# Kernel tuning notes

Measured on AMD Instinct MI355X. Metric: run time of the kernel, lower is better.

The kernel has to match this reference:

```python
import jax, jax.numpy as jnp
import numpy as np

BETA = 0.25


def setup_inputs() -> dict:
    key = jax.random.key(0)
    k1, k2 = jax.random.split(key)
    z = jax.random.normal(k1, (16, 256, 32, 32), dtype=jnp.float32)
    # nn.Embedding init: uniform(-1/K, 1/K) with K = in_channels = 16384
    K, D = 16384, 256
    emb = jax.random.uniform(k2, (K, D), dtype=jnp.float32,
                             minval=-1.0 / K, maxval=1.0 / K)
    return {"z": z, "emb": emb}


def reference(z, emb):
    K, D = emb.shape
    # NCHW -> NHWC, flatten to tokens
    zp = jnp.transpose(z, (0, 2, 3, 1))            # [B,H,W,D]
    zf = zp.reshape(-1, D)                          # [N,D]
    # squared L2 distances: ||z||^2 + ||e||^2 - 2 z.e  -> [N,K]
    d = (jnp.sum(zf * zf, axis=1, keepdims=True)
         + jnp.sum(emb * emb, axis=1)
         - 2.0 * jnp.matmul(zf, emb.T))
    idx = jnp.argmin(d, axis=1)                     # [N] int
    # gather via direct lookup (equivalent to one-hot @ emb)
    z_q = emb[idx].reshape(zp.shape)                # [B,H,W,D]
    # commitment + codebook loss
    loss = (jnp.mean((jax.lax.stop_gradient(z_q) - zp) ** 2)
            + BETA * jnp.mean((z_q - jax.lax.stop_gradient(zp)) ** 2))
    # perplexity from code usage histogram (same as mean of one-hot rows)
    counts = jax.ops.segment_sum(jnp.ones_like(idx, dtype=jnp.float32), idx,
                                 num_segments=K)
    e_mean = counts / idx.shape[0]
    perplexity = jnp.exp(-jnp.sum(e_mean * jnp.log(e_mean + 1e-10)))
    # straight-through estimator, back to NCHW
    z_q_st = zp + jax.lax.stop_gradient(z_q - zp)
    z_q_out = jnp.transpose(z_q_st, (0, 3, 1, 2))   # [B,D,H,W]
    return z_q_out, loss, perplexity, idx
```

## Files before the change

### kernel.cpp

```cpp
#include <hip/hip_runtime.h>
#include <math.h>

#define NTOK   16384
#define DDIM   256
#define HWD    1024
#define CHW    262144
#define MARGIN 3.0e-4f
#define CLIPF  5.5f
#define QS     (127.0f/5.5f)
#define EQS    2080768.0f
#define SCALE  (5.5f/(127.0f*127.0f*16384.0f))

#define WS_TI8   0u
#define WS_CI8   4194304u
#define WS_M1    8388608u
#define WS_M2    16777216u
#define WS_ARG   25165824u
#define WS_FLG   29360128u
#define WS_EE    29376512u
#define WS_ZZ    29442048u
#define WS_IDX   29507584u
#define WS_CNT   29573120u
#define WS_SUM   29638656u

typedef __attribute__((ext_vector_type(4)))  int   i32x4;
typedef __attribute__((ext_vector_type(16))) char  c16;

__device__ __forceinline__ void top2m(int& a1, int& a2, const int b1, const int b2) {
  const int mn = min(a1, b1);
  a1 = max(a1, b1);
  a2 = max(max(a2, b2), mn);
}

__global__ __launch_bounds__(256) void k_prep(const float* __restrict__ z,
                                              const float* __restrict__ emb,
                                              char* __restrict__ Ti8,
                                              char* __restrict__ Ci8,
                                              float* __restrict__ zz,
                                              float* __restrict__ ee,
                                              float* __restrict__ zt,
                                              unsigned char* __restrict__ flags) {
  const int bid = blockIdx.x;
  const int tid = threadIdx.x;
  const int t64 = tid & 63, chunk = tid >> 6;
  if (bid < 256) {
    __shared__ double part[4][64];
    __shared__ int   fpart[4][64];
    const int n = bid * 64 + t64;
    const int b = n >> 10, hw = n & 1023;
    const float* zp = z + (size_t)b * CHW + hw;
    float tmp[64];
    double s = 0.0;
    int clip = 0;
    #pragma unroll
    for (int j = 0; j < 64; ++j) {
      const float f = zp[(size_t)(chunk * 64 + j) * HWD];
      tmp[j] = f;
      s += (double)f * (double)f;
      clip |= (fabsf(f) > CLIPF) ? 1 : 0;
    }
    c16 q[4];
    #pragma unroll
    for (int sl = 0; sl < 4; ++sl)
      #pragma unroll
      for (int j = 0; j < 16; ++j)
        q[sl][j] = (char)(int)rintf(fminf(fmaxf(tmp[sl * 16 + j], -CLIPF), CLIPF) * QS);
    const int rl = n & 127, tile = n >> 7;
    char* dst = Ti8 + (size_t)tile * 32768 + chunk * 8192 + rl * 64;
    const int sw = ((rl >> 1) & 3) << 4;
    #pragma unroll
    for (int sl = 0; sl < 4; ++sl) *(c16*)(dst + ((sl * 16) ^ sw)) = q[sl];
    float* ztp = zt + (size_t)n * 256 + chunk * 64;
    #pragma unroll
    for (int j4 = 0; j4 < 16; ++j4) *(float4*)(ztp + j4 * 4) = *(float4*)&tmp[j4 * 4];
    part[chunk][t64] = s;
    fpart[chunk][t64] = clip;
    __syncthreads();
    if (tid < 64) {
      zz[n] = (float)(part[0][t64] + part[1][t64] + part[2][t64] + part[3][t64]);
      flags[n] = (unsigned char)(fpart[0][t64] | fpart[1][t64] | fpart[2][t64] | fpart[3][t64]);
    }
  } else {
    __shared__ float rows[64][257];
    __shared__ double part2[4][64];
    const int k0 = (bid - 256) * 64;
    for (int i = tid; i < 16384; i += 256)
      rows[i >> 8][i & 255] = emb[(size_t)k0 * DDIM + i];
    __syncthreads();
    const int code = k0 + t64;
    double s = 0.0;
    c16 q[4];
    #pragma unroll
    for (int sl = 0; sl < 4; ++sl)
      #pragma unroll
      for (int j = 0; j < 16; ++j) {
        const float f = rows[t64][chunk * 64 + sl * 16 + j];
        q[sl][j] = (char)(int)rintf(f * EQS);
        s += (double)f * (double)f;
      }
    char* dst = Ci8 + (size_t)code * 256 + chunk * 64;
    #pragma unroll
    for (int sl = 0; sl < 4; ++sl) *(c16*)(dst + sl * 16) = q[sl];
    part2[chunk][t64] = s;
    __syncthreads();
    if (tid < 64)
      ee[code] = (float)(part2[0][t64] + part2[1][t64] + part2[2][t64] + part2[3][t64]);
  }
}

__global__ __launch_bounds__(256) void k_mdist(
    const char* __restrict__ tokimg, const char* __restrict__ codrows,
    _Float16* __restrict__ M1, _Float16* __restrict__ M2,
    unsigned char* __restrict__ ARG) {
  __shared__ __attribute__((aligned(16))) char ldsB[65536];
  __shared__ _Float16 m1l[256];
  __shared__ _Float16 m2l[256];
  __shared__ unsigned char agl[256];
  const int raw = blockIdx.x;
  const int p = raw & 7;
  const int ctile = p * 16 + ((raw >> 3) & 15);
  const int tgrp = raw >> 7;
  const int tid = threadIdx.x;
  const int w = tid >> 6, lane = tid & 63;
  const int wr = w >> 1, wc = w & 1;
  const int fr = lane & 15, fq = lane >> 4;

  i32x4 afr[4][4];
  {
    const char* ab = codrows + (size_t)(ctile * 128 + wr * 64 + fr) * 256 + fq * 16;
    #pragma unroll
    for (int m = 0; m < 4; ++m)
      #pragma unroll
      for (int kc = 0; kc < 4; ++kc)
        afr[m][kc] = *(const i32x4*)(ab + m * 16 * 256 + kc * 64);
  }

  int boff[4][4];
  #pragma unroll
  for (int n = 0; n < 4; ++n)
    #pragma unroll
    for (int kc = 0; kc < 4; ++kc) {
      const int t = wc * 64 + n * 16 + fr;
      boff[n][kc] = kc * 8192 + t * 64 + ((fq * 16) ^ (((t >> 1) & 3) << 4));
    }

  #define STAGEB(buf, tt)                                                             \
    {                                                                                 \
      const char* src = tokimg + (size_t)(tt) * 32768;                                \
      char* dstb = ldsB + (buf) * 32768;                                              \
      _Pragma("unroll")                                                               \
      for (int r = 0; r < 8; ++r) {                                                   \
        const int u = r * 256 + tid;                                                  \
        __builtin_amdgcn_global_load_lds(                                             \
            (const __attribute__((address_space(1))) void*)(src + u * 16),            \
            (__attribute__((address_space(3))) void*)(dstb + u * 16), 16, 0, 0);      \
      }                                                                               \
    }

  STAGEB(0, tgrp * 8);
  __syncthreads();

  const int fq4 = fq * 4;
  for (int it = 0; it < 8; ++it) {
    const int ttile = tgrp * 8 + it;
    if (it < 7) STAGEB((it + 1) & 1, ttile + 1);
    const char* bufb = ldsB + (it & 1) * 32768;

    i32x4 acc[4][4];
    #pragma unroll
    for (int m = 0; m < 4; ++m)
      #pragma unroll
      for (int n = 0; n < 4; ++n) acc[m][n] = (i32x4)0;

    #pragma unroll
    for (int kc = 0; kc < 4; ++kc) {
      i32x4 b[4];
      #pragma unroll
      for (int n = 0; n < 4; ++n) b[n] = *(const i32x4*)(bufb + boff[n][kc]);
      #pragma unroll
      for (int m = 0; m < 4; ++m)
        #pragma unroll
        for (int n = 0; n < 4; ++n)
          acc[m][n] = __builtin_amdgcn_mfma_i32_16x16x64_i8(afr[m][kc], b[n], acc[m][n], 0, 0, 0);
    }

    #pragma unroll
    for (int n = 0; n < 4; ++n) {
      int p1[8], p2[8];
      #pragma unroll
      for (int m = 0; m < 4; ++m)
        #pragma unroll
        for (int jj = 0; jj < 2; ++jj) {
          const int k0 = (acc[m][n][2 * jj]     << 8) | (m * 16 + fq4 + 2 * jj);
          const int k1 = (acc[m][n][2 * jj + 1] << 8) | (m * 16 + fq4 + 2 * jj + 1);
          p1[m * 2 + jj] = max(k0, k1);
          p2[m * 2 + jj] = min(k0, k1);
        }
      top2m(p1[0], p2[0], p1[1], p2[1]); top2m(p1[2], p2[2], p1[3], p2[3]);
      top2m(p1[4], p2[4], p1[5], p2[5]); top2m(p1[6], p2[6], p1[7], p2[7]);
      top2m(p1[0], p2[0], p1[2], p2[2]); top2m(p1[4], p2[4], p1[6], p2[6]);
      top2m(p1[0], p2[0], p1[4], p2[4]);
      int k1 = p1[0], k2 = p2[0];
      #pragma unroll
      for (int off = 16; off <= 32; off <<= 1) {
        const int o1 = __shfl_xor(k1, off, 64);
        const int o2 = __shfl_xor(k2, off, 64);
        top2m(k1, k2, o1, o2);
      }
      if (lane < 16) {
        const int tl = wc * 64 + n * 16 + fr;
        m1l[tl * 2 + wr] = (_Float16)(-2.0f * SCALE * (float)(k1 >> 8));
        m2l[tl * 2 + wr] = (_Float16)(-2.0f * SCALE * (float)(k2 >> 8));
        agl[tl * 2 + wr] = (unsigned char)(k1 & 255);
      }
    }
    __syncthreads();
    if (tid < 128) {
      const int tok = ttile * 128 + tid;
      *(unsigned int*)((char*)M1 + (size_t)tok * 512 + ctile * 4) =
          *(const unsigned int*)(m1l + tid * 2);
      M2[(size_t)(ctile * 2) * NTOK + tok]     = m2l[tid * 2];
      M2[(size_t)(ctile * 2 + 1) * NTOK + tok] = m2l[tid * 2 + 1];
      ARG[(size_t)(ctile * 2) * NTOK + tok]     = agl[tid * 2];
      ARG[(size_t)(ctile * 2 + 1) * NTOK + tok] = agl[tid * 2 + 1];
    }
    __syncthreads();
  }
}

__global__ __launch_bounds__(256) void k_pick(
    const float* __restrict__ zt, const float* __restrict__ emb,
    const float* __restrict__ zz, const float* __restrict__ ee,
    const _Float16* __restrict__ M1, const _Float16* __restrict__ M2,
    const unsigned char* __restrict__ ARG, const unsigned char* __restrict__ flags,
    int* __restrict__ idx, float* __restrict__ out_idxf) {
  __shared__ float zrow[256];
  __shared__ int clist[2048];
  __shared__ int ccnt;
  __shared__ float wm[4];
  __shared__ unsigned long long bests[16];
  const int tid = threadIdx.x;
  const int w = tid >> 6, lane = tid & 63;
  const int g16 = lane >> 4, l16 = lane & 15;
  const int G = w * 4 + g16;
  for (int ni = 0; ni < 8; ++ni) {
    const int n = blockIdx.x * 8 + ni;
    __syncthreads();
    if (tid == 0) ccnt = 0;
    zrow[tid] = zt[(size_t)n * 256 + tid];
    const float ta = (float)M1[(size_t)n * 256 + tid];
    float mr = ta;
    #pragma unroll
    for (int o = 32; o; o >>= 1) mr = fminf(mr, __shfl_xor(mr, o, 64));
    if (lane == 0) wm[w] = mr;
    __syncthreads();
    const int ex0 = flags[n];
    const float thr = ex0 ? 3.0e38f
                          : fminf(fminf(wm[0], wm[1]), fminf(wm[2], wm[3])) + MARGIN;
    if (!ex0 && ta <= thr) {
      const float m2v = (float)M2[(size_t)tid * NTOK + n];
      if (m2v > thr) {
        const int pos = atomicAdd(&ccnt, 1);
        if (pos < 2048) clist[pos] = tid * 64 + (int)ARG[(size_t)tid * NTOK + n];
      } else {
        const int pos = atomicAdd(&ccnt, 64);
        if (pos + 64 <= 2048)
          for (int i = 0; i < 64; ++i) clist[pos + i] = tid * 64 + i;
      }
    }
    __syncthreads();
    const int doEx = ex0 || (ccnt > 2048);
    const int nc = doEx ? 16384 : ccnt;
    const float zzn = zz[n];
    unsigned long long best = ~0ull;
    for (int ci = 0; ci < nc; ci += 16) {
      int k;
      if (doEx) k = ci + G;
      else { const int sl = ci + G; k = clist[sl < nc ? sl : 0]; }
      const float* er = emb + (size_t)k * DDIM;
      double s = 0.0;
      #pragma unroll
      for (int qq = 0; qq < 4; ++qq) {
        const float4 ev = *(const float4*)(er + qq * 64 + l16 * 4);
        const float4 zv = *(const float4*)(&zrow[qq * 64 + l16 * 4]);
        s += (double)zv.x * (double)ev.x + (double)zv.y * (double)ev.y
           + (double)zv.z * (double)ev.z + (double)zv.w * (double)ev.w;
      }
      #pragma unroll
      for (int o = 8; o; o >>= 1) s += __shfl_xor(s, o, 16);
      if (l16 == 0) {
        const float mm = (float)s;
        const float d = (zzn + ee[k]) - 2.0f * mm;
        const unsigned long long c =
            ((unsigned long long)__float_as_uint(d) << 32) | (unsigned int)k;
        if (c < best) best = c;
      }
    }
    if (l16 == 0) bests[G] = best;
    __syncthreads();
    if (tid == 0) {
      unsigned long long bb = bests[0];
      #pragma unroll
      for (int i = 1; i < 16; ++i) bb = bests[i] < bb ? bests[i] : bb;
      const int k0 = (int)(bb & 0xffffffffu);
      idx[n] = k0;
      out_idxf[n] = (float)k0;
    }
  }
}

__global__ __launch_bounds__(256) void k_scatter(
    const float* __restrict__ z, const float* __restrict__ emb,
    const int* __restrict__ idx, float* __restrict__ out_zq,
    int* __restrict__ counts, double* __restrict__ sums) {
  __shared__ float et[64][257];
  __shared__ int sidx[64];
  __shared__ double w4[4];
  const int tg = blockIdx.x;
  const int n0 = tg * 64;
  const int b = n0 >> 10, hw0 = n0 & 1023;
  const int tid = threadIdx.x;
  if (tid < 64) sidx[tid] = idx[n0 + tid];
  __syncthreads();
  for (int i = tid; i < 16384; i += 256) {
    const int t = i >> 8, d = i & 255;
    et[t][d] = emb[(size_t)sidx[t] * DDIM + d];
  }
  __syncthreads();
  const float* zb = z + (size_t)b * CHW + hw0;
  float* ob = out_zq + (size_t)b * CHW + hw0;
  double s = 0.0;
  for (int i = tid; i < 16384; i += 256) {
    const int d = i >> 6, t = i & 63;
    const float v = et[t][d];
    const float diff = v - zb[(size_t)d * HWD + t];
    ob[(size_t)d * HWD + t] = v;
    s += (double)diff * (double)diff;
  }
  #pragma unroll
  for (int o = 32; o; o >>= 1) s += __shfl_xor(s, o, 64);
  const int wd = tid >> 6, lane = tid & 63;
  if (lane == 0) w4[wd] = s;
  __syncthreads();
  if (tid == 0) atomicAdd(&sums[0], w4[0] + w4[1] + w4[2] + w4[3]);
  if (tid < 64) atomicAdd(&counts[sidx[tid]], 1);
}

__global__ __launch_bounds__(256) void k_hist(const int* __restrict__ counts,
                                              double* __restrict__ sums) {
  const int i = blockIdx.x * 256 + threadIdx.x;
  const float em = (float)counts[i] * (1.0f / 16384.0f);
  const float term = em * logf(em + 1e-10f);
  double s = (double)term;
  #pragma unroll
  for (int o = 32; o; o >>= 1) s += __shfl_xor(s, o, 64);
  __shared__ double w4[4];
  const int wid = threadIdx.x >> 6, lane = threadIdx.x & 63;
  if (lane == 0) w4[wid] = s;
  __syncthreads();
  if (threadIdx.x == 0) atomicAdd(&sums[1], w4[0] + w4[1] + w4[2] + w4[3]);
}

__global__ void k_final(const double* __restrict__ sums,
                        float* __restrict__ out_loss,
                        float* __restrict__ out_perp) {
  if (threadIdx.x == 0) {
    out_loss[0] = (float)(1.25 * sums[0] / 4194304.0);
    out_perp[0] = (float)exp(-sums[1]);
  }
}

extern "C" void kernel_launch(void* const* d_in, const int* in_sizes, int n_in,
                              void* d_out, int out_size, void* d_ws, size_t ws_size,
                              hipStream_t stream) {
  const float* z   = (const float*)d_in[0];
  const float* emb = (const float*)d_in[1];
  float* out      = (float*)d_out;
  float* out_zq   = out;
  float* out_loss = out + 4194304;
  float* out_perp = out + 4194305;
  float* out_idxf = out + 4194306;
  float* zt       = out;

  char* ws = (char*)d_ws;
  char* Ti8 = ws + WS_TI8;
  char* Ci8 = ws + WS_CI8;
  _Float16* M1 = (_Float16*)(ws + WS_M1);
  _Float16* M2 = (_Float16*)(ws + WS_M2);
  unsigned char* ARG = (unsigned char*)(ws + WS_ARG);
  unsigned char* flags = (unsigned char*)(ws + WS_FLG);
  float*  ee      = (float*)(ws + WS_EE);
  float*  zz      = (float*)(ws + WS_ZZ);
  int*    idx     = (int*)  (ws + WS_IDX);
  int*    counts  = (int*)  (ws + WS_CNT);
  double* sums    = (double*)(ws + WS_SUM);

  hipMemsetAsync(counts, 0, 65536 + 16, stream);

  k_prep <<<512, 256, 0, stream>>>(z, emb, Ti8, Ci8, zz, ee, zt, flags);
  k_mdist<<<2048, 256, 0, stream>>>(Ti8, Ci8, M1, M2, ARG);
  k_pick <<<2048, 256, 0, stream>>>(zt, emb, zz, ee, M1, M2, ARG, flags, idx, out_idxf);
  k_scatter<<<256, 256, 0, stream>>>(z, emb, idx, out_zq, counts, sums);
  k_hist <<<64, 256, 0, stream>>>(counts, sums);
  k_final<<<1, 64, 0, stream>>>(sums, out_loss, out_perp);
}
```

Before: 208.7 us.

## Halve token tile in distance kernel to raise occupancy and double-buffer epilogue

After: 214.4 us. +2.7%, slower.

```diff
diff --git a/kernel.cpp b/kernel.cpp
--- a/kernel.cpp
+++ b/kernel.cpp
@@ -108,14 +108,14 @@
   }
 }
 
-__global__ __launch_bounds__(256) void k_mdist(
+__global__ __launch_bounds__(256, 4) void k_mdist(
     const char* __restrict__ tokimg, const char* __restrict__ codrows,
     _Float16* __restrict__ M1, _Float16* __restrict__ M2,
     unsigned char* __restrict__ ARG) {
-  __shared__ __attribute__((aligned(16))) char ldsB[65536];
-  __shared__ _Float16 m1l[256];
-  __shared__ _Float16 m2l[256];
-  __shared__ unsigned char agl[256];
+  __shared__ __attribute__((aligned(16))) char ldsB[32768];
+  __shared__ _Float16 m1l[2][128];
+  __shared__ _Float16 m2l[2][128];
+  __shared__ unsigned char agl[2][128];
   const int raw = blockIdx.x;
   const int p = raw & 7;
   const int ctile = p * 16 + ((raw >> 3) & 15);
@@ -135,57 +135,59 @@
         afr[m][kc] = *(const i32x4*)(ab + m * 16 * 256 + kc * 64);
   }
 
-  int boff[4][4];
+  int boff[2][4];
   #pragma unroll
-  for (int n = 0; n < 4; ++n)
+  for (int n = 0; n < 2; ++n)
     #pragma unroll
     for (int kc = 0; kc < 4; ++kc) {
-      const int t = wc * 64 + n * 16 + fr;
-      boff[n][kc] = kc * 8192 + t * 64 + ((fq * 16) ^ (((t >> 1) & 3) << 4));
-    }
-
-  #define STAGEB(buf, tt)                                                             \
+      const int t = wc * 32 + n * 16 + fr;
+      boff[n][kc] = kc * 4096 + t * 64 + ((fq * 16) ^ (((t >> 1) & 3) << 4));
+    }
+
+  #define STAGEB(buf, it)                                                             \
     {                                                                                 \
-      const char* src = tokimg + (size_t)(tt) * 32768;                                \
-      char* dstb = ldsB + (buf) * 32768;                                              \
+      const int ht = tgrp * 16 + (it);                                                \
+      const char* src = tokimg + (size_t)(ht >> 1) * 32768 + (ht & 1) * 4096;         \
+      char* dstb = ldsB + (buf) * 16384;                                              \
       _Pragma("unroll")                                                               \
-      for (int r = 0; r < 8; ++r) {                                                   \
-        const int u = r * 256 + tid;                                                  \
+      for (int r = 0; r < 4; ++r) {                                                   \
         __builtin_amdgcn_global_load_lds(                                             \
-            (const __attribute__((address_space(1))) void*)(src + u * 16),            \
-            (__attribute__((address_space(3))) void*)(dstb + u * 16), 16, 0, 0);      \
+            (const __attribute__((address_space(1))) void*)(src + r * 8192 + tid * 16),\
+            (__attribute__((address_space(3))) void*)(dstb + r * 4096 + tid * 16),    \
+            16, 0, 0);                                                                \
       }                                                                               \
     }
 
-  STAGEB(0, tgrp * 8);
+  STAGEB(0, 0);
   __syncthreads();
 
   const int fq4 = fq * 4;
-  for (int it = 0; it < 8; ++it) {
-    const int ttile = tgrp * 8 + it;
-    if (it < 7) STAGEB((it + 1) & 1, ttile + 1);
-    const char* bufb = ldsB + (it & 1) * 32768;
-
-    i32x4 acc[4][4];
+  #pragma unroll 2
+  for (int it = 0; it < 16; ++it) {
+    const int pb = it & 1;
+    if (it < 15) STAGEB(pb ^ 1, it + 1);
+    const char* bufb = ldsB + pb * 16384;
+
+    i32x4 acc[4][2];
     #pragma unroll
     for (int m = 0; m < 4; ++m)
       #pragma unroll
-      for (int n = 0; n < 4; ++n) acc[m][n] = (i32x4)0;
+      for (int n = 0; n < 2; ++n) acc[m][n] = (i32x4)0;
 
     #pragma unroll
     for (int kc = 0; kc < 4; ++kc) {
-      i32x4 b[4];
-      #pragma unroll
-      for (int n = 0; n < 4; ++n) b[n] = *(const i32x4*)(bufb + boff[n][kc]);
+      i32x4 b[2];
+      #pragma unroll
+      for (int n = 0; n < 2; ++n) b[n] = *(const i32x4*)(bufb + boff[n][kc]);
       #pragma unroll
       for (int m = 0; m < 4; ++m)
         #pragma unroll
-        for (int n = 0; n < 4; ++n)
+        for (int n = 0; n < 2; ++n)
           acc[m][n] = __builtin_amdgcn_mfma_i32_16x16x64_i8(afr[m][kc], b[n], acc[m][n], 0, 0, 0);
     }
 
     #pragma unroll
-    for (int n = 0; n < 4; ++n) {
+    for (int n = 0; n < 2; ++n) {
       int p1[8], p2[8];
       #pragma unroll
       for (int m = 0; m < 4; ++m)
@@ -208,23 +210,32 @@
         top2m(k1, k2, o1, o2);
       }
       if (lane < 16) {
-        const int tl = wc * 64 + n * 16 + fr;
-        m1l[tl * 2 + wr] = (_Float16)(-2.0f * SCALE * (float)(k1 >> 8));
-        m2l[tl * 2 + wr] = (_Float16)(-2.0f * SCALE * (float)(k2 >> 8));
-        agl[tl * 2 + wr] = (unsigned char)(k1 & 255);
-      }
-    }
-    __syncthreads();
-    if (tid < 128) {
-      const int tok = ttile * 128 + tid;
-      *(unsigned int*)((char*)M1 + (size_t)tok * 512 + ctile * 4) =
-          *(const unsigned int*)(m1l + tid * 2);
-      M2[(size_t)(ctile * 2) * NTOK + tok]     = m2l[tid * 2];
-      M2[(size_t)(ctile * 2 + 1) * NTOK + tok] = m2l[tid * 2 + 1];
-      ARG[(size_t)(ctile * 2) * NTOK + tok]     = agl[tid * 2];
-      ARG[(size_t)(ctile * 2 + 1) * NTOK + tok] = agl[tid * 2 + 1];
-    }
-    __syncthreads();
+        const int tl = wc * 32 + n * 16 + fr;
+        m1l[pb][tl * 2 + wr] = (_Float16)(-2.0f * SCALE * (float)(k1 >> 8));
+        m2l[pb][tl * 2 + wr] = (_Float16)(-2.0f * SCALE * (float)(k2 >> 8));
+        agl[pb][tl * 2 + wr] = (unsigned char)(k1 & 255);
+      }
+    }
+    __syncthreads();
+    {
+      const int ht = tgrp * 16 + it;
+      if (tid < 64) {
+        const int tok = ht * 64 + tid;
+        *(unsigned int*)((char*)M1 + (size_t)tok * 512 + ctile * 4) =
+            *(const unsigned int*)(&m1l[pb][tid * 2]);
+      } else if (tid < 192) {
+        const int u = tid - 64;
+        const int tok = ht * 64 + (u >> 1);
+        const int sub = ctile * 2 + (u & 1);
+        M2[(size_t)sub * NTOK + tok] = m2l[pb][(u >> 1) * 2 + (u & 1)];
+      } else {
+        const int u = tid - 192;
+        const int tok = ht * 64 + u;
+        const unsigned short a2 = *(const unsigned short*)(&agl[pb][u * 2]);
+        ARG[(size_t)(ctile * 2) * NTOK + tok]     = (unsigned char)(a2 & 255);
+        ARG[(size_t)(ctile * 2 + 1) * NTOK + tok] = (unsigned char)(a2 >> 8);
+      }
+    }
   }
 }
 
```

## Fuse scatter, loss and histogram into pick kernel; drop zt staging

Applied to the files above, without the earlier changes.

New measurement: 232.2 us. +11.3%, slower.

```diff
diff --git a/kernel.cpp b/kernel.cpp
--- a/kernel.cpp
+++ b/kernel.cpp
@@ -38,7 +38,6 @@
                                               char* __restrict__ Ci8,
                                               float* __restrict__ zz,
                                               float* __restrict__ ee,
-                                              float* __restrict__ zt,
                                               unsigned char* __restrict__ flags) {
   const int bid = blockIdx.x;
   const int tid = threadIdx.x;
@@ -70,9 +69,6 @@
     const int sw = ((rl >> 1) & 3) << 4;
     #pragma unroll
     for (int sl = 0; sl < 4; ++sl) *(c16*)(dst + ((sl * 16) ^ sw)) = q[sl];
-    float* ztp = zt + (size_t)n * 256 + chunk * 64;
-    #pragma unroll
-    for (int j4 = 0; j4 < 16; ++j4) *(float4*)(ztp + j4 * 4) = *(float4*)&tmp[j4 * 4];
     part[chunk][t64] = s;
     fpart[chunk][t64] = clip;
     __syncthreads();
@@ -229,25 +225,38 @@
 }
 
 __global__ __launch_bounds__(256) void k_pick(
-    const float* __restrict__ zt, const float* __restrict__ emb,
+    const float* __restrict__ z, const float* __restrict__ emb,
     const float* __restrict__ zz, const float* __restrict__ ee,
     const _Float16* __restrict__ M1, const _Float16* __restrict__ M2,
     const unsigned char* __restrict__ ARG, const unsigned char* __restrict__ flags,
-    int* __restrict__ idx, float* __restrict__ out_idxf) {
-  __shared__ float zrow[256];
+    float* __restrict__ out_zq, int* __restrict__ counts,
+    double* __restrict__ sums, float* __restrict__ out_idxf) {
+  __shared__ float zr[8][260];
+  __shared__ float er[8][260];
   __shared__ int clist[2048];
   __shared__ int ccnt;
   __shared__ float wm[4];
   __shared__ unsigned long long bests[16];
+  __shared__ int sidx8[8];
+  __shared__ double w4[4];
   const int tid = threadIdx.x;
   const int w = tid >> 6, lane = tid & 63;
   const int g16 = lane >> 4, l16 = lane & 15;
   const int G = w * 4 + g16;
+  const int n0 = blockIdx.x * 8;
+  const int b = n0 >> 10, hw0 = n0 & 1023;
+
+  #pragma unroll
+  for (int r = 0; r < 8; ++r) {
+    const int i2 = r * 256 + tid;
+    const int d = i2 >> 3, t = i2 & 7;
+    zr[t][d] = z[(size_t)b * CHW + (size_t)d * HWD + hw0 + t];
+  }
+
   for (int ni = 0; ni < 8; ++ni) {
-    const int n = blockIdx.x * 8 + ni;
+    const int n = n0 + ni;
     __syncthreads();
     if (tid == 0) ccnt = 0;
-    zrow[tid] = zt[(size_t)n * 256 + tid];
     const float ta = (float)M1[(size_t)n * 256 + tid];
     float mr = ta;
     #pragma unroll
@@ -277,12 +286,12 @@
       int k;
       if (doEx) k = ci + G;
       else { const int sl = ci + G; k = clist[sl < nc ? sl : 0]; }
-      const float* er = emb + (size_t)k * DDIM;
+      const float* erow = emb + (size_t)k * DDIM;
       double s = 0.0;
       #pragma unroll
       for (int qq = 0; qq < 4; ++qq) {
-        const float4 ev = *(const float4*)(er + qq * 64 + l16 * 4);
-        const float4 zv = *(const float4*)(&zrow[qq * 64 + l16 * 4]);
+        const float4 ev = *(const float4*)(erow + qq * 64 + l16 * 4);
+        const float4 zv = *(const float4*)(&zr[ni][qq * 64 + l16 * 4]);
         s += (double)zv.x * (double)ev.x + (double)zv.y * (double)ev.y
            + (double)zv.z * (double)ev.z + (double)zv.w * (double)ev.w;
       }
@@ -303,70 +312,58 @@
       #pragma unroll
       for (int i = 1; i < 16; ++i) bb = bests[i] < bb ? bests[i] : bb;
       const int k0 = (int)(bb & 0xffffffffu);
-      idx[n] = k0;
+      sidx8[ni] = k0;
       out_idxf[n] = (float)k0;
     }
   }
-}
-
-__global__ __launch_bounds__(256) void k_scatter(
-    const float* __restrict__ z, const float* __restrict__ emb,
-    const int* __restrict__ idx, float* __restrict__ out_zq,
-    int* __restrict__ counts, double* __restrict__ sums) {
-  __shared__ float et[64][257];
-  __shared__ int sidx[64];
+  __syncthreads();
+
+  #pragma unroll
+  for (int r = 0; r < 8; ++r) er[r][tid] = emb[(size_t)sidx8[r] * DDIM + tid];
+  __syncthreads();
+
+  double s = 0.0;
+  #pragma unroll
+  for (int r = 0; r < 8; ++r) {
+    const float diff = er[r][tid] - zr[r][tid];
+    s += (double)diff * (double)diff;
+  }
+  #pragma unroll
+  for (int o = 32; o; o >>= 1) s += __shfl_xor(s, o, 64);
+  if (lane == 0) w4[w] = s;
+
+  float* ob = out_zq + (size_t)b * CHW + hw0;
+  #pragma unroll
+  for (int r = 0; r < 8; ++r) {
+    const int i2 = r * 256 + tid;
+    const int d = i2 >> 3, t = i2 & 7;
+    ob[(size_t)d * HWD + t] = er[t][d];
+  }
+  __syncthreads();
+  if (tid == 0) atomicAdd(&sums[0], w4[0] + w4[1] + w4[2] + w4[3]);
+  if (tid < 8) atomicAdd(&counts[sidx8[tid]], 1);
+}
+
+__global__ __launch_bounds__(256) void k_histfinal(const int* __restrict__ counts,
+                                                   const double* __restrict__ sums,
+                                                   float* __restrict__ out_loss,
+                                                   float* __restrict__ out_perp) {
   __shared__ double w4[4];
-  const int tg = blockIdx.x;
-  const int n0 = tg * 64;
-  const int b = n0 >> 10, hw0 = n0 & 1023;
   const int tid = threadIdx.x;
-  if (tid < 64) sidx[tid] = idx[n0 + tid];
-  __syncthreads();
-  for (int i = tid; i < 16384; i += 256) {
-    const int t = i >> 8, d = i & 255;
-    et[t][d] = emb[(size_t)sidx[t] * DDIM + d];
-  }
-  __syncthreads();
-  const float* zb = z + (size_t)b * CHW + hw0;
-  float* ob = out_zq + (size_t)b * CHW + hw0;
   double s = 0.0;
   for (int i = tid; i < 16384; i += 256) {
-    const int d = i >> 6, t = i & 63;
-    const float v = et[t][d];
-    const float diff = v - zb[(size_t)d * HWD + t];
-    ob[(size_t)d * HWD + t] = v;
-    s += (double)diff * (double)diff;
+    const float em = (float)counts[i] * (1.0f / 16384.0f);
+    s += (double)(em * logf(em + 1e-10f));
   }
   #pragma unroll
   for (int o = 32; o; o >>= 1) s += __shfl_xor(s, o, 64);
-  const int wd = tid >> 6, lane = tid & 63;
-  if (lane == 0) w4[wd] = s;
-  __syncthreads();
-  if (tid == 0) atomicAdd(&sums[0], w4[0] + w4[1] + w4[2] + w4[3]);
-  if (tid < 64) atomicAdd(&counts[sidx[tid]], 1);
-}
-
-__global__ __launch_bounds__(256) void k_hist(const int* __restrict__ counts,
-                                              double* __restrict__ sums) {
-  const int i = blockIdx.x * 256 + threadIdx.x;
-  const float em = (float)counts[i] * (1.0f / 16384.0f);
-  const float term = em * logf(em + 1e-10f);
-  double s = (double)term;
-  #pragma unroll
-  for (int o = 32; o; o >>= 1) s += __shfl_xor(s, o, 64);
-  __shared__ double w4[4];
-  const int wid = threadIdx.x >> 6, lane = threadIdx.x & 63;
+  const int wid = tid >> 6, lane = tid & 63;
   if (lane == 0) w4[wid] = s;
   __syncthreads();
-  if (threadIdx.x == 0) atomicAdd(&sums[1], w4[0] + w4[1] + w4[2] + w4[3]);
-}
-
-__global__ void k_final(const double* __restrict__ sums,
-                        float* __restrict__ out_loss,
-                        float* __restrict__ out_perp) {
-  if (threadIdx.x == 0) {
+  if (tid == 0) {
+    const double S = w4[0] + w4[1] + w4[2] + w4[3];
     out_loss[0] = (float)(1.25 * sums[0] / 4194304.0);
-    out_perp[0] = (float)exp(-sums[1]);
+    out_perp[0] = (float)exp(-S);
   }
 }
 
@@ -380,7 +377,6 @@
   float* out_loss = out + 4194304;
   float* out_perp = out + 4194305;
   float* out_idxf = out + 4194306;
-  float* zt       = out;
 
   char* ws = (char*)d_ws;
   char* Ti8 = ws + WS_TI8;
@@ -391,16 +387,14 @@
   unsigned char* flags = (unsigned char*)(ws + WS_FLG);
   float*  ee      = (float*)(ws + WS_EE);
   float*  zz      = (float*)(ws + WS_ZZ);
-  int*    idx     = (int*)  (ws + WS_IDX);
   int*    counts  = (int*)  (ws + WS_CNT);
   double* sums    = (double*)(ws + WS_SUM);
 
   hipMemsetAsync(counts, 0, 65536 + 16, stream);
 
-  k_prep <<<512, 256, 0, stream>>>(z, emb, Ti8, Ci8, zz, ee, zt, flags);
+  k_prep <<<512, 256, 0, stream>>>(z, emb, Ti8, Ci8, zz, ee, flags);
   k_mdist<<<2048, 256, 0, stream>>>(Ti8, Ci8, M1, M2, ARG);
-  k_pick <<<2048, 256, 0, stream>>>(zt, emb, zz, ee, M1, M2, ARG, flags, idx, out_idxf);
-  k_scatter<<<256, 256, 0, stream>>>(z, emb, idx, out_zq, counts, sums);
-  k_hist <<<64, 256, 0, stream>>>(counts, sums);
-  k_final<<<1, 64, 0, stream>>>(sums, out_loss, out_perp);
-}
+  k_pick <<<2048, 256, 0, stream>>>(z, emb, zz, ee, M1, M2, ARG, flags,
+                                    out_zq, counts, sums, out_idxf);
+  k_histfinal<<<1, 256, 0, stream>>>(counts, sums, out_loss, out_perp);
+}
```

## Assign one token per wavefront in k_pick and fuse histogram with final kernel

Applied to the files above, without the earlier changes.

New measurement: 207.7 us. No clear change (-0.5%).

```diff
diff --git a/kernel.cpp b/kernel.cpp
--- a/kernel.cpp
+++ b/kernel.cpp
@@ -25,6 +25,7 @@
 
 typedef __attribute__((ext_vector_type(4)))  int   i32x4;
 typedef __attribute__((ext_vector_type(16))) char  c16;
+typedef __attribute__((ext_vector_type(4)))  _Float16 h4;
 
 __device__ __forceinline__ void top2m(int& a1, int& a2, const int b1, const int b2) {
   const int mn = min(a1, b1);
@@ -234,55 +235,57 @@
     const _Float16* __restrict__ M1, const _Float16* __restrict__ M2,
     const unsigned char* __restrict__ ARG, const unsigned char* __restrict__ flags,
     int* __restrict__ idx, float* __restrict__ out_idxf) {
-  __shared__ float zrow[256];
-  __shared__ int clist[2048];
-  __shared__ int ccnt;
-  __shared__ float wm[4];
-  __shared__ unsigned long long bests[16];
+  __shared__ float zrow[4][260];
+  __shared__ int   clist[4][576];
+  __shared__ int   wcnt[4];
   const int tid = threadIdx.x;
   const int w = tid >> 6, lane = tid & 63;
   const int g16 = lane >> 4, l16 = lane & 15;
-  const int G = w * 4 + g16;
-  for (int ni = 0; ni < 8; ++ni) {
-    const int n = blockIdx.x * 8 + ni;
-    __syncthreads();
-    if (tid == 0) ccnt = 0;
-    zrow[tid] = zt[(size_t)n * 256 + tid];
-    const float ta = (float)M1[(size_t)n * 256 + tid];
-    float mr = ta;
+  for (int ni = 0; ni < 2; ++ni) {
+    const int n = blockIdx.x * 8 + w * 2 + ni;
+    if (lane == 0) wcnt[w] = 0;
+    *(float4*)&zrow[w][lane * 4] = *(const float4*)(zt + (size_t)n * 256 + lane * 4);
+    const h4 mv = *(const h4*)(M1 + (size_t)n * 256 + lane * 4);
+    float ta4[4];
+    #pragma unroll
+    for (int s = 0; s < 4; ++s) ta4[s] = (float)mv[s];
+    float mr = fminf(fminf(ta4[0], ta4[1]), fminf(ta4[2], ta4[3]));
     #pragma unroll
     for (int o = 32; o; o >>= 1) mr = fminf(mr, __shfl_xor(mr, o, 64));
-    if (lane == 0) wm[w] = mr;
-    __syncthreads();
     const int ex0 = flags[n];
-    const float thr = ex0 ? 3.0e38f
-                          : fminf(fminf(wm[0], wm[1]), fminf(wm[2], wm[3])) + MARGIN;
-    if (!ex0 && ta <= thr) {
-      const float m2v = (float)M2[(size_t)tid * NTOK + n];
-      if (m2v > thr) {
-        const int pos = atomicAdd(&ccnt, 1);
-        if (pos < 2048) clist[pos] = tid * 64 + (int)ARG[(size_t)tid * NTOK + n];
-      } else {
-        const int pos = atomicAdd(&ccnt, 64);
-        if (pos + 64 <= 2048)
-          for (int i = 0; i < 64; ++i) clist[pos + i] = tid * 64 + i;
-      }
-    }
-    __syncthreads();
-    const int doEx = ex0 || (ccnt > 2048);
-    const int nc = doEx ? 16384 : ccnt;
+    const float thr = ex0 ? 3.0e38f : mr + MARGIN;
+    if (!ex0) {
+      #pragma unroll
+      for (int s = 0; s < 4; ++s) {
+        if (ta4[s] <= thr) {
+          const int sub = lane * 4 + s;
+          const float m2v = (float)M2[(size_t)sub * NTOK + n];
+          if (m2v > thr) {
+            const int pos = atomicAdd(&wcnt[w], 1);
+            if (pos < 576) clist[w][pos] = sub * 64 + (int)ARG[(size_t)sub * NTOK + n];
+          } else {
+            const int pos = atomicAdd(&wcnt[w], 64);
+            if (pos + 64 <= 576)
+              for (int i = 0; i < 64; ++i) clist[w][pos + i] = sub * 64 + i;
+          }
+        }
+      }
+    }
+    const int cnt = wcnt[w];
+    const int doEx = ex0 || (cnt > 576);
+    const int nc = doEx ? 16384 : cnt;
     const float zzn = zz[n];
     unsigned long long best = ~0ull;
-    for (int ci = 0; ci < nc; ci += 16) {
+    for (int ci = 0; ci < nc; ci += 4) {
       int k;
-      if (doEx) k = ci + G;
-      else { const int sl = ci + G; k = clist[sl < nc ? sl : 0]; }
-      const float* er = emb + (size_t)k * DDIM;
+      if (doEx) k = ci + g16;
+      else { const int sl = ci + g16; k = clist[w][sl < cnt ? sl : 0]; }
+      const float* erow = emb + (size_t)k * DDIM;
       double s = 0.0;
       #pragma unroll
       for (int qq = 0; qq < 4; ++qq) {
-        const float4 ev = *(const float4*)(er + qq * 64 + l16 * 4);
-        const float4 zv = *(const float4*)(&zrow[qq * 64 + l16 * 4]);
+        const float4 ev = *(const float4*)(erow + qq * 64 + l16 * 4);
+        const float4 zv = *(const float4*)(&zrow[w][qq * 64 + l16 * 4]);
         s += (double)zv.x * (double)ev.x + (double)zv.y * (double)ev.y
            + (double)zv.z * (double)ev.z + (double)zv.w * (double)ev.w;
       }
@@ -296,13 +299,15 @@
         if (c < best) best = c;
       }
     }
-    if (l16 == 0) bests[G] = best;
-    __syncthreads();
-    if (tid == 0) {
-      unsigned long long bb = bests[0];
-      #pragma unroll
-      for (int i = 1; i < 16; ++i) bb = bests[i] < bb ? bests[i] : bb;
-      const int k0 = (int)(bb & 0xffffffffu);
+    unsigned long long b0 = (l16 == 0) ? best : ~0ull;
+    {
+      const unsigned long long o1 = __shfl_xor(b0, 16, 64);
+      b0 = o1 < b0 ? o1 : b0;
+      const unsigned long long o2 = __shfl_xor(b0, 32, 64);
+      b0 = o2 < b0 ? o2 : b0;
+    }
+    if (lane == 0) {
+      const int k0 = (int)(b0 & 0xffffffffu);
       idx[n] = k0;
       out_idxf[n] = (float)k0;
     }
@@ -346,27 +351,26 @@
   if (tid < 64) atomicAdd(&counts[sidx[tid]], 1);
 }
 
-__global__ __launch_bounds__(256) void k_hist(const int* __restrict__ counts,
-                                              double* __restrict__ sums) {
-  const int i = blockIdx.x * 256 + threadIdx.x;
-  const float em = (float)counts[i] * (1.0f / 16384.0f);
-  const float term = em * logf(em + 1e-10f);
-  double s = (double)term;
+__global__ __launch_bounds__(256) void k_histfinal(const int* __restrict__ counts,
+                                                   const double* __restrict__ sums,
+                                                   float* __restrict__ out_loss,
+                                                   float* __restrict__ out_perp) {
+  __shared__ double w4[4];
+  const int tid = threadIdx.x;
+  double s = 0.0;
+  for (int i = tid; i < 16384; i += 256) {
+    const float em = (float)counts[i] * (1.0f / 16384.0f);
+    s += (double)(em * logf(em + 1e-10f));
+  }
   #pragma unroll
   for (int o = 32; o; o >>= 1) s += __shfl_xor(s, o, 64);
-  __shared__ double w4[4];
-  const int wid = threadIdx.x >> 6, lane = threadIdx.x & 63;
+  const int wid = tid >> 6, lane = tid & 63;
   if (lane == 0) w4[wid] = s;
   __syncthreads();
-  if (threadIdx.x == 0) atomicAdd(&sums[1], w4[0] + w4[1] + w4[2] + w4[3]);
-}
-
-__global__ void k_final(const double* __restrict__ sums,
-                        float* __restrict__ out_loss,
-                        float* __restrict__ out_perp) {
-  if (threadIdx.x == 0) {
+  if (tid == 0) {
+    const double S = w4[0] + w4[1] + w4[2] + w4[3];
     out_loss[0] = (float)(1.25 * sums[0] / 4194304.0);
-    out_perp[0] = (float)exp(-sums[1]);
+    out_perp[0] = (float)exp(-S);
   }
 }
 
@@ -401,6 +405,5 @@
   k_mdist<<<2048, 256, 0, stream>>>(Ti8, Ci8, M1, M2, ARG);
   k_pick <<<2048, 256, 0, stream>>>(zt, emb, zz, ee, M1, M2, ARG, flags, idx, out_idxf);
   k_scatter<<<256, 256, 0, stream>>>(z, emb, idx, out_zq, counts, sums);
-  k_hist <<<64, 256, 0, stream>>>(counts, sums);
-  k_final<<<1, 64, 0, stream>>>(sums, out_loss, out_perp);
-}
+  k_histfinal<<<1, 256, 0, stream>>>(counts, sums, out_loss, out_perp);
+}
```
